# Performance work log

Hardware: AMD Instinct MI355X
Metric: run time of the kernel (lower is better)

The kernel has to match this reference:

```python
import jax, jax.numpy as jnp
import numpy as np

B, S, D, H = 4, 2048, 256, 8
SPARSITY = 0.1


def setup_inputs() -> dict:
    key = jax.random.key(0)
    ks = jax.random.split(key, 6)
    s = 0.02
    return {
        "x": jax.random.normal(ks[0], (B, S, D), jnp.float32),
        # nn.MultiheadAttention packed in-projection (W_q;W_k;W_v) and out-projection
        "w_in": jax.random.normal(ks[1], (3 * D, D), jnp.float32) * s,
        "b_in": jnp.zeros((3 * D,), jnp.float32),
        "w_out": jax.random.normal(ks[2], (D, D), jnp.float32) * s,
        "b_out": jnp.zeros((D,), jnp.float32),
        # sparsity gate: Linear(D, D//4) -> ReLU -> Linear(D//4, 1) -> Sigmoid
        "gate_w1": jax.random.normal(ks[3], (D // 4, D), jnp.float32) * s,
        "gate_b1": jnp.zeros((D // 4,), jnp.float32),
        "gate_w2": jax.random.normal(ks[4], (1, D // 4), jnp.float32) * s,
        "gate_b2": jnp.zeros((1,), jnp.float32),
    }


def reference(x, w_in, b_in, w_out, b_out, gate_w1, gate_b1, gate_w2, gate_b2):
    b, s, d = x.shape
    hd = d // H

    # --- adaptive sparse mask (top-k importance gating) ---
    h = jax.nn.relu(jnp.einsum('bsd,fd->bsf', x, gate_w1) + gate_b1)
    importance = jax.nn.sigmoid(jnp.einsum('bsf,of->bso', h, gate_w2) + gate_b2)[..., 0]  # [B,S]
    k = max(1, int(s * SPARSITY))
    _, top_idx = jax.lax.top_k(importance, k)  # [B,k]
    keep = jnp.zeros((b, s), dtype=bool).at[jnp.arange(b)[:, None], top_idx].set(True)  # [B,S]

    # --- multi-head attention with key_padding_mask = ~keep ---
    qkv = jnp.einsum('bsd,ed->bse', x, w_in) + b_in  # [B,S,3D]
    q, kk, v = jnp.split(qkv, 3, axis=-1)
    split_heads = lambda t: t.reshape(b, s, H, hd).transpose(0, 2, 1, 3)  # [B,H,S,hd]
    q, kk, v = split_heads(q), split_heads(kk), split_heads(v)

    scores = jnp.einsum('bhqd,bhkd->bhqk', q, kk) / jnp.sqrt(jnp.asarray(hd, x.dtype))
    neg = jnp.finfo(scores.dtype).min
    scores = jnp.where(keep[:, None, None, :], scores, neg)  # mask non-selected keys
    attn = jax.nn.softmax(scores, axis=-1)

    out = jnp.einsum('bhqk,bhkd->bhqd', attn, v)
    out = out.transpose(0, 2, 1, 3).reshape(b, s, d)
    return jnp.einsum('bsd,od->bso', out, w_out) + b_out
```

## Files before the change

kernel.cpp:

```cpp
#include <hip/hip_runtime.h>
#include <hip/hip_bf16.h>

#define B_  4
#define S_  2048
#define D_  256
#define H_  8
#define HD_ 32
#define K_  204
#define SCALE_ 0.17677669529663687f

#define OFF_IMP    0
#define OFF_KG     8192
#define OFF_VG     112640
#define OFF_META   217088
#define OFF_KIDX   217104
#define OFF_Q      218368
#define OFF_XH     1266944
#define OFF_XL     2315520
#define OFF_AOH    3364096
#define OFF_AOL    4412672
#define OFF_WQH    5461248
#define OFF_WQL    5494016
#define OFF_WOH    5526784
#define OFF_WOL    5559552

#define GSTR 80
#define PSTR 228
#define VSTR 228

typedef __attribute__((ext_vector_type(8))) short short8v;
typedef __attribute__((ext_vector_type(4))) float f32x4;
typedef unsigned short ushort_t;

static __device__ __forceinline__ unsigned short f2bf(float f) {
    unsigned int u = __float_as_uint(f);
    u += 0x7FFFu + ((u >> 16) & 1u);
    return (unsigned short)(u >> 16);
}
static __device__ __forceinline__ float bf2f(unsigned short h) {
    return __uint_as_float((unsigned int)h << 16);
}
static __device__ __forceinline__ short8v ld_bf8(const unsigned short* p) {
    union { unsigned int u[4]; short8v v; } cv;
    const uint2 a  = *(const uint2*)(p);
    const uint2 b2 = *(const uint2*)(p + 4);
    cv.u[0] = a.x; cv.u[1] = a.y; cv.u[2] = b2.x; cv.u[3] = b2.y;
    return cv.v;
}
static __device__ __forceinline__ void split_store8(
    const float* __restrict__ src, unsigned short* dh, unsigned short* dl)
{
    short8v h, l;
    #pragma unroll
    for (int e = 0; e < 8; ++e) {
        const float f = src[e];
        const unsigned short hh = f2bf(f);
        h[e] = (short)hh;
        l[e] = (short)f2bf(f - bf2f(hh));
    }
    *(short8v*)dh = h;
    *(short8v*)dl = l;
}

__global__ __launch_bounds__(256) void gate_kernel(
    const float* __restrict__ x, const float* __restrict__ gw1,
    const float* __restrict__ gb1, const float* __restrict__ gw2,
    const float* __restrict__ w_in, const float* __restrict__ w_out, float* ws)
{
    const int t0 = blockIdx.x * 8;
    const int tid = threadIdx.x;
    __shared__ __align__(16) float xs[8 * D_];
    __shared__ float hred[8 * 64];

    const float4* src = (const float4*)(x + (size_t)t0 * D_);
    ((float4*)xs)[tid]       = src[tid];
    ((float4*)xs)[tid + 256] = src[tid + 256];
    __syncthreads();

    {
        unsigned short* XH = (unsigned short*)(ws + OFF_XH);
        unsigned short* XL = (unsigned short*)(ws + OFF_XL);
        split_store8(xs + tid * 8, XH + (size_t)t0 * D_ + tid * 8,
                                   XL + (size_t)t0 * D_ + tid * 8);
    }
    if (blockIdx.x < 64) {
        const int e0 = blockIdx.x * 2048 + tid * 8;
        if (e0 < 65536) {
            split_store8(w_in + e0, (unsigned short*)(ws + OFF_WQH) + e0,
                                    (unsigned short*)(ws + OFF_WQL) + e0);
        } else {
            const int e = e0 - 65536;
            split_store8(w_out + e, (unsigned short*)(ws + OFF_WOH) + e,
                                    (unsigned short*)(ws + OFF_WOL) + e);
        }
    }
    if (blockIdx.x == 0 && tid < 8) ((int*)(ws + OFF_META))[tid] = 0;

    const int c = tid & 3, f = tid >> 2;
    float4 wv[16];
    const float4* wr = (const float4*)(gw1 + (size_t)f * D_) + c;
    #pragma unroll
    for (int j = 0; j < 16; ++j) wv[j] = wr[j * 4];
    const float bb = gb1[f], g2 = gw2[f];

    #pragma unroll
    for (int tk = 0; tk < 8; ++tk) {
        const float4* xr = (const float4*)(xs + tk * D_) + c;
        float a = 0.0f;
        #pragma unroll
        for (int j = 0; j < 16; ++j) {
            float4 xv = xr[j * 4];
            a += wv[j].x*xv.x + wv[j].y*xv.y + wv[j].z*xv.z + wv[j].w*xv.w;
        }
        a += __shfl_xor(a, 1);
        a += __shfl_xor(a, 2);
        if (c == 0) hred[tk * 64 + f] = fmaxf(a + bb, 0.0f) * g2;
    }
    __syncthreads();

    const int tk = tid >> 5, ln = tid & 31;
    float s = hred[tk * 64 + ln] + hred[tk * 64 + ln + 32];
    #pragma unroll
    for (int o = 16; o; o >>= 1) s += __shfl_xor(s, o, 32);
    if (ln == 0) ws[OFF_IMP + t0 + tk] = s;
}

__global__ __launch_bounds__(256) void rank_kernel(
    const float* __restrict__ ws_imp, int* kidx, int* meta)
{
    const int b  = blockIdx.x >> 7;
    const int ic = blockIdx.x & 127;
    const int tid = threadIdx.x;
    __shared__ __align__(16) float vs[S_];
    const float* src = ws_imp + b * S_;
    #pragma unroll
    for (int cc = 0; cc < 2; ++cc)
        ((float4*)vs)[tid + cc*256] = ((const float4*)src)[tid + cc*256];
    __syncthreads();

    const int il = tid >> 4;
    const int c  = tid & 15;
    const int i  = ic * 16 + il;
    const float vi = vs[i];
    int gt = 0, eq = 0;
    const float4* v4 = (const float4*)vs + c * 32;
    #pragma unroll 8
    for (int t = 0; t < 32; ++t) {
        const int j4 = (t + c) & 31;
        float4 w = v4[j4];
        const int base = c * 128 + j4 * 4;
        gt += (w.x > vi); eq += (w.x == vi) && (base + 0 < i);
        gt += (w.y > vi); eq += (w.y == vi) && (base + 1 < i);
        gt += (w.z > vi); eq += (w.z == vi) && (base + 2 < i);
        gt += (w.w > vi); eq += (w.w == vi) && (base + 3 < i);
    }
    int r = gt + eq;
    r += __shfl_xor(r, 1);
    r += __shfl_xor(r, 2);
    r += __shfl_xor(r, 4);
    r += __shfl_xor(r, 8);
    if (c == 0 && r < K_) {
        const int p = atomicAdd(&meta[2 + b], 1);
        kidx[b * K_ + p] = i;
    }
}

__global__ __launch_bounds__(256) void kv_kernel(
    const float* __restrict__ x, const float* __restrict__ w_in,
    const float* __restrict__ b_in, unsigned short* __restrict__ KG,
    unsigned short* __restrict__ VG, const int* __restrict__ kidx)
{
    const int b = blockIdx.y, j0 = blockIdx.x * 4, tid = threadIdx.x;
    __shared__ __align__(16) float xs[4 * D_];
    __shared__ int toks[4];
    if (tid < 4) {
        int tk = kidx[b * K_ + j0 + tid];
        toks[tid] = min(max(tk, 0), S_ - 1);
    }
    __syncthreads();
    {
        const int kk = tid >> 6, l = tid & 63;
        ((float4*)xs)[kk * 64 + l] =
            ((const float4*)(x + ((size_t)b * S_ + toks[kk]) * D_))[l];
    }
    __syncthreads();

    const int c = tid & 3, f = tid >> 2;
    #pragma unroll 1
    for (int fg = 0; fg < 8; ++fg) {
        const int eh = fg * 64 + f;
        float4 wv[16];
        const float4* wr = (const float4*)(w_in + (size_t)(D_ + eh) * D_) + c;
        #pragma unroll
        for (int j = 0; j < 16; ++j) wv[j] = wr[j * 4];
        float a0 = 0, a1 = 0, a2 = 0, a3 = 0;
        #pragma unroll
        for (int j = 0; j < 16; ++j) {
            float4 w = wv[j];
            float4 x0 = ((const float4*)(xs + 0*D_))[c + j*4];
            float4 x1 = ((const float4*)(xs + 1*D_))[c + j*4];
            float4 x2 = ((const float4*)(xs + 2*D_))[c + j*4];
            float4 x3 = ((const float4*)(xs + 3*D_))[c + j*4];
            a0 += w.x*x0.x + w.y*x0.y + w.z*x0.z + w.w*x0.w;
            a1 += w.x*x1.x + w.y*x1.y + w.z*x1.z + w.w*x1.w;
            a2 += w.x*x2.x + w.y*x2.y + w.z*x2.z + w.w*x2.w;
            a3 += w.x*x3.x + w.y*x3.y + w.z*x3.z + w.w*x3.w;
        }
        a0 += __shfl_xor(a0, 1); a0 += __shfl_xor(a0, 2);
        a1 += __shfl_xor(a1, 1); a1 += __shfl_xor(a1, 2);
        a2 += __shfl_xor(a2, 1); a2 += __shfl_xor(a2, 2);
        a3 += __shfl_xor(a3, 1); a3 += __shfl_xor(a3, 2);
        if (c == 0) {
            const float bias = b_in[D_ + eh];
            const int isV = eh >> 8;
            const int ee = eh & 255;
            const int h = ee >> 5, d = ee & 31;
            unsigned short* dst = (isV ? VG : KG) + ((b * H_ + h) * K_) * HD_ + d;
            dst[(j0 + 0) * HD_] = f2bf(a0 + bias);
            dst[(j0 + 1) * HD_] = f2bf(a1 + bias);
            dst[(j0 + 2) * HD_] = f2bf(a2 + bias);
            dst[(j0 + 3) * HD_] = f2bf(a3 + bias);
        }
    }
}

template<bool QOUT>
__global__ __launch_bounds__(256) void gemm_kernel(
    const unsigned short* __restrict__ Ah, const unsigned short* __restrict__ Al,
    const unsigned short* __restrict__ Bh, const unsigned short* __restrict__ Bl,
    const float* __restrict__ bias, float* __restrict__ Cf,
    unsigned short* __restrict__ Cq)
{
    __shared__ __align__(16) unsigned short Ash[64 * GSTR];
    __shared__ __align__(16) unsigned short Asl[64 * GSTR];
    __shared__ __align__(16) unsigned short Bsh[64 * GSTR];
    __shared__ __align__(16) unsigned short Bsl[64 * GSTR];

    const int tid = threadIdx.x;
    const int m0 = blockIdx.x * 64, n0 = blockIdx.y * 64;
    const int lane = tid & 63, w = tid >> 6;
    const int c = lane & 15, g = lane >> 4;
    const int mq = w >> 1, nq = w & 1;

    const f32x4 zf = {0.0f, 0.0f, 0.0f, 0.0f};
    f32x4 acc[2][2] = {{zf, zf}, {zf, zf}};

    const int srow = tid >> 2, sseg = tid & 3;
    const unsigned short* Aph = Ah + (size_t)(m0 + srow) * D_ + sseg * 16;
    const unsigned short* Apl = Al + (size_t)(m0 + srow) * D_ + sseg * 16;
    const unsigned short* Bph = Bh + (size_t)(n0 + srow) * D_ + sseg * 16;
    const unsigned short* Bpl = Bl + (size_t)(n0 + srow) * D_ + sseg * 16;

    short8v arh[2], arl[2], brh[2], brl[2];
    #pragma unroll
    for (int u = 0; u < 2; ++u) {
        arh[u] = *(const short8v*)(Aph + u*8); arl[u] = *(const short8v*)(Apl + u*8);
        brh[u] = *(const short8v*)(Bph + u*8); brl[u] = *(const short8v*)(Bpl + u*8);
    }

    for (int k0 = 0; k0 < D_; k0 += 64) {
        __syncthreads();
        #pragma unroll
        for (int u = 0; u < 2; ++u) {
            *(short8v*)&Ash[srow*GSTR + sseg*16 + u*8] = arh[u];
            *(short8v*)&Asl[srow*GSTR + sseg*16 + u*8] = arl[u];
            *(short8v*)&Bsh[srow*GSTR + sseg*16 + u*8] = brh[u];
            *(short8v*)&Bsl[srow*GSTR + sseg*16 + u*8] = brl[u];
        }
        __syncthreads();
        if (k0 + 64 < D_) {
            #pragma unroll
            for (int u = 0; u < 2; ++u) {
                arh[u] = *(const short8v*)(Aph + k0 + 64 + u*8);
                arl[u] = *(const short8v*)(Apl + k0 + 64 + u*8);
                brh[u] = *(const short8v*)(Bph + k0 + 64 + u*8);
                brl[u] = *(const short8v*)(Bpl + k0 + 64 + u*8);
            }
        }
        #pragma unroll
        for (int ks = 0; ks < 2; ++ks) {
            short8v am[2][2], bm[2][2];
            #pragma unroll
            for (int t = 0; t < 2; ++t) {
                const int ra = (mq*32 + t*16 + c) * GSTR + ks*32 + g*8;
                am[t][0] = *(const short8v*)&Ash[ra];
                am[t][1] = *(const short8v*)&Asl[ra];
                const int rb = (nq*32 + t*16 + c) * GSTR + ks*32 + g*8;
                bm[t][0] = *(const short8v*)&Bsh[rb];
                bm[t][1] = *(const short8v*)&Bsl[rb];
            }
            #pragma unroll
            for (int mt = 0; mt < 2; ++mt)
                #pragma unroll
                for (int nt = 0; nt < 2; ++nt) {
                    acc[mt][nt] = __builtin_amdgcn_mfma_f32_16x16x32_bf16(am[mt][0], bm[nt][0], acc[mt][nt], 0, 0, 0);
                    acc[mt][nt] = __builtin_amdgcn_mfma_f32_16x16x32_bf16(am[mt][0], bm[nt][1], acc[mt][nt], 0, 0, 0);
                    acc[mt][nt] = __builtin_amdgcn_mfma_f32_16x16x32_bf16(am[mt][1], bm[nt][0], acc[mt][nt], 0, 0, 0);
                }
        }
    }
    #pragma unroll
    for (int nt = 0; nt < 2; ++nt) {
        const int n = n0 + nq*32 + nt*16 + c;
        const float bv = bias[n];
        #pragma unroll
        for (int mt = 0; mt < 2; ++mt) {
            const int m = m0 + mq*32 + mt*16 + g*4;
            #pragma unroll
            for (int r = 0; r < 4; ++r) {
                const float v = acc[mt][nt][r] + bv;
                if (QOUT) Cq[(size_t)(m + r) * D_ + n] = f2bf(v);
                else      Cf[(size_t)(m + r) * D_ + n] = v;
            }
        }
    }
}

__global__ __launch_bounds__(256) void attn_kernel(
    const unsigned short* __restrict__ KG, const unsigned short* __restrict__ VG,
    const unsigned short* __restrict__ Qb,
    unsigned short* __restrict__ aoh, unsigned short* __restrict__ aol)
{
    const int b = blockIdx.z, h = blockIdx.y, q0 = blockIdx.x * 32;
    const int tid = threadIdx.x;
    const int lane = tid & 63, w = tid >> 6;
    const int c = lane & 15, g = lane >> 4;

    __shared__ __align__(16) unsigned short Pl[32 * PSTR];
    __shared__ __align__(16) unsigned short VTl[32 * VSTR];
    __shared__ float redl[4 * 32];
    __shared__ float invl[32];

    const size_t bh = (size_t)(b * H_ + h) * K_ * HD_;
    const unsigned short* KGb = KG + bh;
    const unsigned short* VGb = VG + bh;

    for (int i = tid; i < K_ * 4; i += 256) {
        const int j = i >> 2, dc = i & 3;
        const short8v v = *(const short8v*)(VGb + i * 8);
        #pragma unroll
        for (int r = 0; r < 8; ++r)
            VTl[(dc*8 + r)*VSTR + j] = (unsigned short)v[r];
    }
    {
        const int q = tid >> 3, cc = tid & 7;
        *(unsigned int*)&Pl[q * PSTR + 208 + cc * 2] = 0u;
    }
    for (int i = tid; i < 32 * 20; i += 256) {
        VTl[(i / 20) * VSTR + 204 + (i % 20)] = 0;
    }

    short8v qa[2];
    #pragma unroll
    for (int qt = 0; qt < 2; ++qt)
        qa[qt] = *(const short8v*)(Qb + (size_t)(b * S_ + q0 + qt*16 + c) * D_ + h * HD_ + g * 8);

    const int njt = (w == 0) ? 4 : 3;
    f32x4 acc[2][4];
    const f32x4 zf = {0.0f, 0.0f, 0.0f, 0.0f};
    #pragma unroll
    for (int qt = 0; qt < 2; ++qt)
        #pragma unroll
        for (int t = 0; t < 4; ++t) acc[qt][t] = zf;

    for (int t = 0; t < njt; ++t) {
        const int jt = w + 4 * t;
        const int jc = min(jt * 16 + c, K_ - 1);
        const short8v kb = *(const short8v*)(KGb + (size_t)jc * HD_ + g * 8);
        acc[0][t] = __builtin_amdgcn_mfma_f32_16x16x32_bf16(qa[0], kb, acc[0][t], 0, 0, 0);
        acc[1][t] = __builtin_amdgcn_mfma_f32_16x16x32_bf16(qa[1], kb, acc[1][t], 0, 0, 0);
    }

    float rs[2][4] = {{0,0,0,0},{0,0,0,0}};
    for (int t = 0; t < njt; ++t) {
        const int jg = (w + 4 * t) * 16 + c;
        const bool val = (jg < K_);
        #pragma unroll
        for (int qt = 0; qt < 2; ++qt) {
            #pragma unroll
            for (int r = 0; r < 4; ++r) {
                const float e = val ? __expf(acc[qt][t][r] * SCALE_) : 0.0f;
                rs[qt][r] += e;
                Pl[(qt*16 + g*4 + r) * PSTR + jg] = f2bf(e);
            }
        }
    }
    #pragma unroll
    for (int qt = 0; qt < 2; ++qt)
        #pragma unroll
        for (int r = 0; r < 4; ++r) {
            float s = rs[qt][r];
            s += __shfl_xor(s, 1); s += __shfl_xor(s, 2);
            s += __shfl_xor(s, 4); s += __shfl_xor(s, 8);
            if (c == 0) redl[w * 32 + qt*16 + g*4 + r] = s;
        }

    __syncthreads();
    if (tid < 32)
        invl[tid] = 1.0f / (redl[tid] + redl[32 + tid] + redl[64 + tid] + redl[96 + tid]);
    __syncthreads();

    const int dt = w >> 1, qt2 = w & 1;
    f32x4 o = zf;
    const unsigned short* vb = &VTl[(dt*16 + c) * VSTR];
    const unsigned short* pb = &Pl[(qt2*16 + c) * PSTR];
    #pragma unroll
    for (int kt = 0; kt < 7; ++kt) {
        const short8v av = ld_bf8(vb + kt*32 + g*8);
        const short8v bv = ld_bf8(pb + kt*32 + g*8);
        o = __builtin_amdgcn_mfma_f32_16x16x32_bf16(av, bv, o, 0, 0, 0);
    }
    const float iv = invl[qt2*16 + c];
    const size_t oidx = (size_t)(b * S_ + q0 + qt2*16 + c) * D_ + h * HD_ + dt*16 + g*4;
    ushort4 hh, ll;
    {
        const float v0 = o[0]*iv, v1 = o[1]*iv, v2 = o[2]*iv, v3 = o[3]*iv;
        hh.x = f2bf(v0); ll.x = f2bf(v0 - bf2f(hh.x));
        hh.y = f2bf(v1); ll.y = f2bf(v1 - bf2f(hh.y));
        hh.z = f2bf(v2); ll.z = f2bf(v2 - bf2f(hh.z));
        hh.w = f2bf(v3); ll.w = f2bf(v3 - bf2f(hh.w));
    }
    *(ushort4*)(aoh + oidx) = hh;
    *(ushort4*)(aol + oidx) = ll;
}

extern "C" void kernel_launch(void* const* d_in, const int* in_sizes, int n_in,
                              void* d_out, int out_size, void* d_ws, size_t ws_size,
                              hipStream_t stream)
{
    const float* x     = (const float*)d_in[0];
    const float* w_in  = (const float*)d_in[1];
    const float* b_in  = (const float*)d_in[2];
    const float* w_out = (const float*)d_in[3];
    const float* b_out = (const float*)d_in[4];
    const float* gw1   = (const float*)d_in[5];
    const float* gb1   = (const float*)d_in[6];
    const float* gw2   = (const float*)d_in[7];

    float* ws = (float*)d_ws;
    int* meta = (int*)(ws + OFF_META);
    int* kidx = (int*)(ws + OFF_KIDX);
    unsigned short* KG  = (unsigned short*)(ws + OFF_KG);
    unsigned short* VG  = (unsigned short*)(ws + OFF_VG);
    unsigned short* Qb  = (unsigned short*)(ws + OFF_Q);
    unsigned short* XH  = (unsigned short*)(ws + OFF_XH);
    unsigned short* XL  = (unsigned short*)(ws + OFF_XL);
    unsigned short* AOH = (unsigned short*)(ws + OFF_AOH);
    unsigned short* AOL = (unsigned short*)(ws + OFF_AOL);
    unsigned short* WQH = (unsigned short*)(ws + OFF_WQH);
    unsigned short* WQL = (unsigned short*)(ws + OFF_WQL);
    unsigned short* WOH = (unsigned short*)(ws + OFF_WOH);
    unsigned short* WOL = (unsigned short*)(ws + OFF_WOL);
    float* out = (float*)d_out;

    gate_kernel<<<B_ * S_ / 8, 256, 0, stream>>>(x, gw1, gb1, gw2, w_in, w_out, ws);
    rank_kernel<<<B_ * 128, 256, 0, stream>>>(ws + OFF_IMP, kidx, meta);
    kv_kernel<<<dim3(51, B_), 256, 0, stream>>>(x, w_in, b_in, KG, VG, kidx);
    gemm_kernel<true><<<dim3(B_ * S_ / 64, D_ / 64), 256, 0, stream>>>(
        XH, XL, WQH, WQL, b_in, nullptr, Qb);
    attn_kernel<<<dim3(S_ / 32, H_, B_), 256, 0, stream>>>(KG, VG, Qb, AOH, AOL);
    gemm_kernel<false><<<dim3(B_ * S_ / 64, D_ / 64), 256, 0, stream>>>(
        AOH, AOL, WOH, WOL, b_out, out, nullptr);
}
```

Baseline: 163.6 us.

## Compute gathered K/V projection with split-bf16 MFMA GEMM over selected tokens

Replaces the scalar FP32 kv_kernel with a GEMM kernel that gathers the top-k token rows of the pre-split bf16 hi/lo x and runs MFMA against the pre-split K/V weights. The gate kernel now splits all of w_in (not just W_q) into hi/lo halves, and K and V are written to one interleaved [B,K,512] buffer that the attention kernel reads with strided per-head loads. This aims to remove the slow FP32 dot-product path and cut the number of K/V blocks. In exchange, the split precision scheme replaces exact FP32 for K/V, the gate kernel does more weight conversion work, and attention's K/V loads become strided.

Measured after the change: 146.1 us. 10.7% less time.

```diff
diff --git a/kernel.cpp b/kernel.cpp
--- a/kernel.cpp
+++ b/kernel.cpp
@@ -10,19 +10,18 @@
 #define SCALE_ 0.17677669529663687f
 
 #define OFF_IMP    0
-#define OFF_KG     8192
-#define OFF_VG     112640
-#define OFF_META   217088
-#define OFF_KIDX   217104
-#define OFF_Q      218368
-#define OFF_XH     1266944
-#define OFF_XL     2315520
-#define OFF_AOH    3364096
-#define OFF_AOL    4412672
-#define OFF_WQH    5461248
-#define OFF_WQL    5494016
-#define OFF_WOH    5526784
-#define OFF_WOL    5559552
+#define OFF_META   8192
+#define OFF_KIDX   8208
+#define OFF_KV     9232
+#define OFF_Q      218128
+#define OFF_XH     1266704
+#define OFF_XL     2315280
+#define OFF_AOH    3363856
+#define OFF_AOL    4412432
+#define OFF_WIH    5461008
+#define OFF_WIL    5559312
+#define OFF_WOH    5657616
+#define OFF_WOL    5690384
 
 #define GSTR 80
 #define PSTR 228
@@ -30,7 +29,6 @@
 
 typedef __attribute__((ext_vector_type(8))) short short8v;
 typedef __attribute__((ext_vector_type(4))) float f32x4;
-typedef unsigned short ushort_t;
 
 static __device__ __forceinline__ unsigned short f2bf(float f) {
     unsigned int u = __float_as_uint(f);
@@ -83,18 +81,18 @@
         split_store8(xs + tid * 8, XH + (size_t)t0 * D_ + tid * 8,
                                    XL + (size_t)t0 * D_ + tid * 8);
     }
-    if (blockIdx.x < 64) {
+    if (blockIdx.x < 128) {
         const int e0 = blockIdx.x * 2048 + tid * 8;
-        if (e0 < 65536) {
-            split_store8(w_in + e0, (unsigned short*)(ws + OFF_WQH) + e0,
-                                    (unsigned short*)(ws + OFF_WQL) + e0);
+        if (e0 < 196608) {
+            split_store8(w_in + e0, (unsigned short*)(ws + OFF_WIH) + e0,
+                                    (unsigned short*)(ws + OFF_WIL) + e0);
         } else {
-            const int e = e0 - 65536;
+            const int e = e0 - 196608;
             split_store8(w_out + e, (unsigned short*)(ws + OFF_WOH) + e,
                                     (unsigned short*)(ws + OFF_WOL) + e);
         }
     }
-    if (blockIdx.x == 0 && tid < 8) ((int*)(ws + OFF_META))[tid] = 0;
+    if (blockIdx.x == 0 && tid < 16) ((int*)(ws + OFF_META))[tid] = 0;
 
     const int c = tid & 3, f = tid >> 2;
     float4 wv[16];
@@ -165,71 +163,11 @@
     }
 }
 
-__global__ __launch_bounds__(256) void kv_kernel(
-    const float* __restrict__ x, const float* __restrict__ w_in,
-    const float* __restrict__ b_in, unsigned short* __restrict__ KG,
-    unsigned short* __restrict__ VG, const int* __restrict__ kidx)
-{
-    const int b = blockIdx.y, j0 = blockIdx.x * 4, tid = threadIdx.x;
-    __shared__ __align__(16) float xs[4 * D_];
-    __shared__ int toks[4];
-    if (tid < 4) {
-        int tk = kidx[b * K_ + j0 + tid];
-        toks[tid] = min(max(tk, 0), S_ - 1);
-    }
-    __syncthreads();
-    {
-        const int kk = tid >> 6, l = tid & 63;
-        ((float4*)xs)[kk * 64 + l] =
-            ((const float4*)(x + ((size_t)b * S_ + toks[kk]) * D_))[l];
-    }
-    __syncthreads();
-
-    const int c = tid & 3, f = tid >> 2;
-    #pragma unroll 1
-    for (int fg = 0; fg < 8; ++fg) {
-        const int eh = fg * 64 + f;
-        float4 wv[16];
-        const float4* wr = (const float4*)(w_in + (size_t)(D_ + eh) * D_) + c;
-        #pragma unroll
-        for (int j = 0; j < 16; ++j) wv[j] = wr[j * 4];
-        float a0 = 0, a1 = 0, a2 = 0, a3 = 0;
-        #pragma unroll
-        for (int j = 0; j < 16; ++j) {
-            float4 w = wv[j];
-            float4 x0 = ((const float4*)(xs + 0*D_))[c + j*4];
-            float4 x1 = ((const float4*)(xs + 1*D_))[c + j*4];
-            float4 x2 = ((const float4*)(xs + 2*D_))[c + j*4];
-            float4 x3 = ((const float4*)(xs + 3*D_))[c + j*4];
-            a0 += w.x*x0.x + w.y*x0.y + w.z*x0.z + w.w*x0.w;
-            a1 += w.x*x1.x + w.y*x1.y + w.z*x1.z + w.w*x1.w;
-            a2 += w.x*x2.x + w.y*x2.y + w.z*x2.z + w.w*x2.w;
-            a3 += w.x*x3.x + w.y*x3.y + w.z*x3.z + w.w*x3.w;
-        }
-        a0 += __shfl_xor(a0, 1); a0 += __shfl_xor(a0, 2);
-        a1 += __shfl_xor(a1, 1); a1 += __shfl_xor(a1, 2);
-        a2 += __shfl_xor(a2, 1); a2 += __shfl_xor(a2, 2);
-        a3 += __shfl_xor(a3, 1); a3 += __shfl_xor(a3, 2);
-        if (c == 0) {
-            const float bias = b_in[D_ + eh];
-            const int isV = eh >> 8;
-            const int ee = eh & 255;
-            const int h = ee >> 5, d = ee & 31;
-            unsigned short* dst = (isV ? VG : KG) + ((b * H_ + h) * K_) * HD_ + d;
-            dst[(j0 + 0) * HD_] = f2bf(a0 + bias);
-            dst[(j0 + 1) * HD_] = f2bf(a1 + bias);
-            dst[(j0 + 2) * HD_] = f2bf(a2 + bias);
-            dst[(j0 + 3) * HD_] = f2bf(a3 + bias);
-        }
-    }
-}
-
-template<bool QOUT>
-__global__ __launch_bounds__(256) void gemm_kernel(
-    const unsigned short* __restrict__ Ah, const unsigned short* __restrict__ Al,
-    const unsigned short* __restrict__ Bh, const unsigned short* __restrict__ Bl,
-    const float* __restrict__ bias, float* __restrict__ Cf,
-    unsigned short* __restrict__ Cq)
+__global__ __launch_bounds__(256) void kvg_kernel(
+    const unsigned short* __restrict__ XH, const unsigned short* __restrict__ XL,
+    const unsigned short* __restrict__ WKH, const unsigned short* __restrict__ WKL,
+    const float* __restrict__ b_in, unsigned short* __restrict__ KV,
+    const int* __restrict__ kidx)
 {
     __shared__ __align__(16) unsigned short Ash[64 * GSTR];
     __shared__ __align__(16) unsigned short Asl[64 * GSTR];
@@ -237,7 +175,8 @@
     __shared__ __align__(16) unsigned short Bsl[64 * GSTR];
 
     const int tid = threadIdx.x;
-    const int m0 = blockIdx.x * 64, n0 = blockIdx.y * 64;
+    const int b = blockIdx.y;
+    const int m0 = (blockIdx.x & 3) * 64, n0 = (blockIdx.x >> 2) * 64;
     const int lane = tid & 63, w = tid >> 6;
     const int c = lane & 15, g = lane >> 4;
     const int mq = w >> 1, nq = w & 1;
@@ -246,10 +185,11 @@
     f32x4 acc[2][2] = {{zf, zf}, {zf, zf}};
 
     const int srow = tid >> 2, sseg = tid & 3;
-    const unsigned short* Aph = Ah + (size_t)(m0 + srow) * D_ + sseg * 16;
-    const unsigned short* Apl = Al + (size_t)(m0 + srow) * D_ + sseg * 16;
-    const unsigned short* Bph = Bh + (size_t)(n0 + srow) * D_ + sseg * 16;
-    const unsigned short* Bpl = Bl + (size_t)(n0 + srow) * D_ + sseg * 16;
+    const int tok = kidx[b * K_ + min(m0 + srow, K_ - 1)];
+    const unsigned short* Aph = XH + ((size_t)b * S_ + tok) * D_ + sseg * 16;
+    const unsigned short* Apl = XL + ((size_t)b * S_ + tok) * D_ + sseg * 16;
+    const unsigned short* Bph = WKH + (size_t)(n0 + srow) * D_ + sseg * 16;
+    const unsigned short* Bpl = WKL + (size_t)(n0 + srow) * D_ + sseg * 16;
 
     short8v arh[2], arl[2], brh[2], brl[2];
     #pragma unroll
@@ -302,6 +242,96 @@
     #pragma unroll
     for (int nt = 0; nt < 2; ++nt) {
         const int n = n0 + nq*32 + nt*16 + c;
+        const float bv = b_in[D_ + n];
+        #pragma unroll
+        for (int mt = 0; mt < 2; ++mt) {
+            const int j = m0 + mq*32 + mt*16 + g*4;
+            #pragma unroll
+            for (int r = 0; r < 4; ++r)
+                if (j + r < K_)
+                    KV[((size_t)b * K_ + j + r) * 512 + n] = f2bf(acc[mt][nt][r] + bv);
+        }
+    }
+}
+
+template<bool QOUT>
+__global__ __launch_bounds__(256) void gemm_kernel(
+    const unsigned short* __restrict__ Ah, const unsigned short* __restrict__ Al,
+    const unsigned short* __restrict__ Bh, const unsigned short* __restrict__ Bl,
+    const float* __restrict__ bias, float* __restrict__ Cf,
+    unsigned short* __restrict__ Cq)
+{
+    __shared__ __align__(16) unsigned short Ash[64 * GSTR];
+    __shared__ __align__(16) unsigned short Asl[64 * GSTR];
+    __shared__ __align__(16) unsigned short Bsh[64 * GSTR];
+    __shared__ __align__(16) unsigned short Bsl[64 * GSTR];
+
+    const int tid = threadIdx.x;
+    const int m0 = blockIdx.x * 64, n0 = blockIdx.y * 64;
+    const int lane = tid & 63, w = tid >> 6;
+    const int c = lane & 15, g = lane >> 4;
+    const int mq = w >> 1, nq = w & 1;
+
+    const f32x4 zf = {0.0f, 0.0f, 0.0f, 0.0f};
+    f32x4 acc[2][2] = {{zf, zf}, {zf, zf}};
+
+    const int srow = tid >> 2, sseg = tid & 3;
+    const unsigned short* Aph = Ah + (size_t)(m0 + srow) * D_ + sseg * 16;
+    const unsigned short* Apl = Al + (size_t)(m0 + srow) * D_ + sseg * 16;
+    const unsigned short* Bph = Bh + (size_t)(n0 + srow) * D_ + sseg * 16;
+    const unsigned short* Bpl = Bl + (size_t)(n0 + srow) * D_ + sseg * 16;
+
+    short8v arh[2], arl[2], brh[2], brl[2];
+    #pragma unroll
+    for (int u = 0; u < 2; ++u) {
+        arh[u] = *(const short8v*)(Aph + u*8); arl[u] = *(const short8v*)(Apl + u*8);
+        brh[u] = *(const short8v*)(Bph + u*8); brl[u] = *(const short8v*)(Bpl + u*8);
+    }
+
+    for (int k0 = 0; k0 < D_; k0 += 64) {
+        __syncthreads();
+        #pragma unroll
+        for (int u = 0; u < 2; ++u) {
+            *(short8v*)&Ash[srow*GSTR + sseg*16 + u*8] = arh[u];
+            *(short8v*)&Asl[srow*GSTR + sseg*16 + u*8] = arl[u];
+            *(short8v*)&Bsh[srow*GSTR + sseg*16 + u*8] = brh[u];
+            *(short8v*)&Bsl[srow*GSTR + sseg*16 + u*8] = brl[u];
+        }
+        __syncthreads();
+        if (k0 + 64 < D_) {
+            #pragma unroll
+            for (int u = 0; u < 2; ++u) {
+                arh[u] = *(const short8v*)(Aph + k0 + 64 + u*8);
+                arl[u] = *(const short8v*)(Apl + k0 + 64 + u*8);
+                brh[u] = *(const short8v*)(Bph + k0 + 64 + u*8);
+                brl[u] = *(const short8v*)(Bpl + k0 + 64 + u*8);
+            }
+        }
+        #pragma unroll
+        for (int ks = 0; ks < 2; ++ks) {
+            short8v am[2][2], bm[2][2];
+            #pragma unroll
+            for (int t = 0; t < 2; ++t) {
+                const int ra = (mq*32 + t*16 + c) * GSTR + ks*32 + g*8;
+                am[t][0] = *(const short8v*)&Ash[ra];
+                am[t][1] = *(const short8v*)&Asl[ra];
+                const int rb = (nq*32 + t*16 + c) * GSTR + ks*32 + g*8;
+                bm[t][0] = *(const short8v*)&Bsh[rb];
+                bm[t][1] = *(const short8v*)&Bsl[rb];
+            }
+            #pragma unroll
+            for (int mt = 0; mt < 2; ++mt)
+                #pragma unroll
+                for (int nt = 0; nt < 2; ++nt) {
+                    acc[mt][nt] = __builtin_amdgcn_mfma_f32_16x16x32_bf16(am[mt][0], bm[nt][0], acc[mt][nt], 0, 0, 0);
+                    acc[mt][nt] = __builtin_amdgcn_mfma_f32_16x16x32_bf16(am[mt][0], bm[nt][1], acc[mt][nt], 0, 0, 0);
+                    acc[mt][nt] = __builtin_amdgcn_mfma_f32_16x16x32_bf16(am[mt][1], bm[nt][0], acc[mt][nt], 0, 0, 0);
+                }
+        }
+    }
+    #pragma unroll
+    for (int nt = 0; nt < 2; ++nt) {
+        const int n = n0 + nq*32 + nt*16 + c;
         const float bv = bias[n];
         #pragma unroll
         for (int mt = 0; mt < 2; ++mt) {
@@ -317,8 +347,7 @@
 }
 
 __global__ __launch_bounds__(256) void attn_kernel(
-    const unsigned short* __restrict__ KG, const unsigned short* __restrict__ VG,
-    const unsigned short* __restrict__ Qb,
+    const unsigned short* __restrict__ KV, const unsigned short* __restrict__ Qb,
     unsigned short* __restrict__ aoh, unsigned short* __restrict__ aol)
 {
     const int b = blockIdx.z, h = blockIdx.y, q0 = blockIdx.x * 32;
@@ -331,13 +360,11 @@
     __shared__ float redl[4 * 32];
     __shared__ float invl[32];
 
-    const size_t bh = (size_t)(b * H_ + h) * K_ * HD_;
-    const unsigned short* KGb = KG + bh;
-    const unsigned short* VGb = VG + bh;
+    const unsigned short* KVb = KV + (size_t)b * K_ * 512;
 
     for (int i = tid; i < K_ * 4; i += 256) {
         const int j = i >> 2, dc = i & 3;
-        const short8v v = *(const short8v*)(VGb + i * 8);
+        const short8v v = *(const short8v*)(KVb + (size_t)j * 512 + 256 + h * HD_ + dc * 8);
         #pragma unroll
         for (int r = 0; r < 8; ++r)
             VTl[(dc*8 + r)*VSTR + j] = (unsigned short)v[r];
@@ -366,7 +393,7 @@
     for (int t = 0; t < njt; ++t) {
         const int jt = w + 4 * t;
         const int jc = min(jt * 16 + c, K_ - 1);
-        const short8v kb = *(const short8v*)(KGb + (size_t)jc * HD_ + g * 8);
+        const short8v kb = *(const short8v*)(KVb + (size_t)jc * 512 + h * HD_ + g * 8);
         acc[0][t] = __builtin_amdgcn_mfma_f32_16x16x32_bf16(qa[0], kb, acc[0][t], 0, 0, 0);
         acc[1][t] = __builtin_amdgcn_mfma_f32_16x16x32_bf16(qa[1], kb, acc[1][t], 0, 0, 0);
     }
@@ -440,25 +467,25 @@
     float* ws = (float*)d_ws;
     int* meta = (int*)(ws + OFF_META);
     int* kidx = (int*)(ws + OFF_KIDX);
-    unsigned short* KG  = (unsigned short*)(ws + OFF_KG);
-    unsigned short* VG  = (unsigned short*)(ws + OFF_VG);
+    unsigned short* KV  = (unsigned short*)(ws + OFF_KV);
     unsigned short* Qb  = (unsigned short*)(ws + OFF_Q);
     unsigned short* XH  = (unsigned short*)(ws + OFF_XH);
     unsigned short* XL  = (unsigned short*)(ws + OFF_XL);
     unsigned short* AOH = (unsigned short*)(ws + OFF_AOH);
     unsigned short* AOL = (unsigned short*)(ws + OFF_AOL);
-    unsigned short* WQH = (unsigned short*)(ws + OFF_WQH);
-    unsigned short* WQL = (unsigned short*)(ws + OFF_WQL);
+    unsigned short* WIH = (unsigned short*)(ws + OFF_WIH);
+    unsigned short* WIL = (unsigned short*)(ws + OFF_WIL);
     unsigned short* WOH = (unsigned short*)(ws + OFF_WOH);
     unsigned short* WOL = (unsigned short*)(ws + OFF_WOL);
     float* out = (float*)d_out;
 
     gate_kernel<<<B_ * S_ / 8, 256, 0, stream>>>(x, gw1, gb1, gw2, w_in, w_out, ws);
     rank_kernel<<<B_ * 128, 256, 0, stream>>>(ws + OFF_IMP, kidx, meta);
-    kv_kernel<<<dim3(51, B_), 256, 0, stream>>>(x, w_in, b_in, KG, VG, kidx);
+    kvg_kernel<<<dim3(32, B_), 256, 0, stream>>>(
+        XH, XL, WIH + 65536, WIL + 65536, b_in, KV, kidx);
     gemm_kernel<true><<<dim3(B_ * S_ / 64, D_ / 64), 256, 0, stream>>>(
-        XH, XL, WQH, WQL, b_in, nullptr, Qb);
-    attn_kernel<<<dim3(S_ / 32, H_, B_), 256, 0, stream>>>(KG, VG, Qb, AOH, AOL);
+        XH, XL, WIH, WIL, b_in, nullptr, Qb);
+    attn_kernel<<<dim3(S_ / 32, H_, B_), 256, 0, stream>>>(KV, Qb, AOH, AOL);
     gemm_kernel<false><<<dim3(B_ * S_ / 64, D_ / 64), 256, 0, stream>>>(
         AOH, AOL, WOH, WOL, b_out, out, nullptr);
 }
```
